# Optimization experiments

Hardware: AMD Instinct MI355X
Metric: run time of the kernel (lower is better)

Reference implementation:

```python
import jax, jax.numpy as jnp
import numpy as np

B, T, IN, H, OUT = 16384, 32, 64, 512, 19


def setup_inputs() -> dict:
    key = jax.random.key(0)
    ks = jax.random.split(key, 10)
    s = 0.05
    return {
        "input_data": jax.random.normal(ks[0], (B, T, IN), dtype=jnp.float32),
        "Wx0": jax.random.normal(ks[1], (IN, 4 * H), dtype=jnp.float32) * s,
        "Wh0": jax.random.normal(ks[2], (H, 4 * H), dtype=jnp.float32) * s,
        "b0": jnp.zeros((4 * H,), dtype=jnp.float32),
        "Wx1": jax.random.normal(ks[3], (H + 1, 4 * H), dtype=jnp.float32) * s,
        "Wh1": jax.random.normal(ks[4], (H, 4 * H), dtype=jnp.float32) * s,
        "b1": jnp.zeros((4 * H,), dtype=jnp.float32),
        "Wlin": jax.random.normal(ks[5], (H, OUT), dtype=jnp.float32) * s,
        "blin": jnp.zeros((OUT,), dtype=jnp.float32),
        "time_step": T,
    }


def _lstm_gates(x, h, c, Wx, Wh, b):
    # PyTorch LSTMCell gate order: i, f, g, o
    g = x @ Wx + h @ Wh + b
    i, f, gc, o = jnp.split(g, 4, axis=-1)
    cn = jax.nn.sigmoid(f) * c + jax.nn.sigmoid(i) * jnp.tanh(gc)
    hn = jax.nn.sigmoid(o) * jnp.tanh(cn)
    return hn, cn


def reference(input_data, Wx0, Wh0, b0, Wx1, Wh1, b1, Wlin, blin, time_step):
    batch = input_data.shape[0]
    hidden = Wh0.shape[0]

    def step(carry, x_t):
        h0, c0, h1, c1 = carry
        flag = x_t[:, :1]  # condition flag in feature column 0
        # cell 1: condition-gated LSTM update
        h0n, c0n = _lstm_gates(x_t, h0, c0, Wx0, Wh0, b0)
        h0 = flag * h0n + (1.0 - flag) * h0
        c0 = flag * c0n + (1.0 - flag) * c0
        # cell 2 input: [flag, h0]
        x2 = jnp.concatenate([flag, h0], axis=1)
        h1n, c1n = _lstm_gates(x2, h1, c1, Wx1, Wh1, b1)
        h1 = flag * h1n + (1.0 - flag) * h1
        c1 = flag * c1n + (1.0 - flag) * c1
        return (h0, c0, h1, c1), None

    z = jnp.zeros((batch, hidden), dtype=input_data.dtype)
    xs = jnp.swapaxes(input_data[:, :time_step, :], 0, 1)  # [T, B, IN]
    (h0, c0, h1, c1), _ = jax.lax.scan(step, (z, z, z, z), xs)
    return h1 @ Wlin + blin
```

## Files before the change

kernel.cpp:

```cpp
#include <hip/hip_runtime.h>
#include <hip/hip_bf16.h>


#define T_STEPS 32
#define IN_F    64
#define HID     512
#define OUT_F   19
#define BW      64

typedef short bf16x8 __attribute__((ext_vector_type(8)));
typedef float f32x4  __attribute__((ext_vector_type(4)));

__device__ __forceinline__ float fast_sig(float x) {
    return __builtin_amdgcn_rcpf(1.0f + __expf(-x));
}
__device__ __forceinline__ float fast_tanh(float x) {
    return 1.0f - 2.0f * __builtin_amdgcn_rcpf(1.0f + __expf(2.0f * x));
}

#define LBAR() do { \
    asm volatile("s_waitcnt lgkmcnt(0)" ::: "memory"); \
    __builtin_amdgcn_sched_barrier(0); \
    __builtin_amdgcn_s_barrier(); \
    __builtin_amdgcn_sched_barrier(0); \
} while (0)

#define MFMA16(A0, A1, A2, A3, Q0, Q1, Q2, Q3) do { \
    acc[0][0] = __builtin_amdgcn_mfma_f32_16x16x32_bf16(A0, Q0, acc[0][0], 0, 0, 0); \
    acc[1][0] = __builtin_amdgcn_mfma_f32_16x16x32_bf16(A1, Q0, acc[1][0], 0, 0, 0); \
    acc[2][0] = __builtin_amdgcn_mfma_f32_16x16x32_bf16(A2, Q0, acc[2][0], 0, 0, 0); \
    acc[3][0] = __builtin_amdgcn_mfma_f32_16x16x32_bf16(A3, Q0, acc[3][0], 0, 0, 0); \
    acc[0][1] = __builtin_amdgcn_mfma_f32_16x16x32_bf16(A0, Q1, acc[0][1], 0, 0, 0); \
    acc[1][1] = __builtin_amdgcn_mfma_f32_16x16x32_bf16(A1, Q1, acc[1][1], 0, 0, 0); \
    acc[2][1] = __builtin_amdgcn_mfma_f32_16x16x32_bf16(A2, Q1, acc[2][1], 0, 0, 0); \
    acc[3][1] = __builtin_amdgcn_mfma_f32_16x16x32_bf16(A3, Q1, acc[3][1], 0, 0, 0); \
    acc[0][2] = __builtin_amdgcn_mfma_f32_16x16x32_bf16(A0, Q2, acc[0][2], 0, 0, 0); \
    acc[1][2] = __builtin_amdgcn_mfma_f32_16x16x32_bf16(A1, Q2, acc[1][2], 0, 0, 0); \
    acc[2][2] = __builtin_amdgcn_mfma_f32_16x16x32_bf16(A2, Q2, acc[2][2], 0, 0, 0); \
    acc[3][2] = __builtin_amdgcn_mfma_f32_16x16x32_bf16(A3, Q2, acc[3][2], 0, 0, 0); \
    acc[0][3] = __builtin_amdgcn_mfma_f32_16x16x32_bf16(A0, Q3, acc[0][3], 0, 0, 0); \
    acc[1][3] = __builtin_amdgcn_mfma_f32_16x16x32_bf16(A1, Q3, acc[1][3], 0, 0, 0); \
    acc[2][3] = __builtin_amdgcn_mfma_f32_16x16x32_bf16(A2, Q3, acc[2][3], 0, 0, 0); \
    acc[3][3] = __builtin_amdgcn_mfma_f32_16x16x32_bf16(A3, Q3, acc[3][3], 0, 0, 0); \
} while (0)

__global__ void wprep_kernel(const float* __restrict__ src,
                             __hip_bfloat16* __restrict__ dst,
                             int kcBits, int rowOff) {
    int idx = blockIdx.x * 256 + threadIdx.x;
    int total = 2048 << (kcBits + 5);
    if (idx >= total) return;
    int e   = idx & 7;
    int lq  = (idx >> 3) & 3;
    int l15 = (idx >> 5) & 15;
    int kc  = (idx >> 9) & ((1 << kcBits) - 1);
    int cb  = idx >> (9 + kcBits);
    int k   = kc * 32 + lq * 8 + e + rowOff;
    int col = cb * 16 + l15;
    dst[idx] = __float2bfloat16(src[(size_t)k * 2048 + col]);
}

template<int KC, int RTS>
__device__ __forceinline__ void gemm_sec4(const char* aE, const char* aO,
                                          const __hip_bfloat16* b0p,
                                          const __hip_bfloat16* b1p,
                                          const __hip_bfloat16* b2p,
                                          const __hip_bfloat16* b3p,
                                          f32x4 acc[4][4]) {
    bf16x8 pa0, pa1, pa2, pa3, pb0, pb1, pb2, pb3, a0, a1, a2, a3;
    pa0 = *(const bf16x8*)(b0p);
    pa1 = *(const bf16x8*)(b1p);
    pa2 = *(const bf16x8*)(b2p);
    pa3 = *(const bf16x8*)(b3p);
    #pragma unroll 1
    for (int m = 0; m < KC - 2; m += 2) {
        const int ao = (m >> 1) * 128;
        pb0 = *(const bf16x8*)(b0p + (m + 1) * 512);
        pb1 = *(const bf16x8*)(b1p + (m + 1) * 512);
        pb2 = *(const bf16x8*)(b2p + (m + 1) * 512);
        pb3 = *(const bf16x8*)(b3p + (m + 1) * 512);
        a0 = *(const bf16x8*)(aE + ao);
        a1 = *(const bf16x8*)(aE + RTS + ao);
        a2 = *(const bf16x8*)(aE + 2 * RTS + ao);
        a3 = *(const bf16x8*)(aE + 3 * RTS + ao);
        MFMA16(a0, a1, a2, a3, pa0, pa1, pa2, pa3);
        pa0 = *(const bf16x8*)(b0p + (m + 2) * 512);
        pa1 = *(const bf16x8*)(b1p + (m + 2) * 512);
        pa2 = *(const bf16x8*)(b2p + (m + 2) * 512);
        pa3 = *(const bf16x8*)(b3p + (m + 2) * 512);
        a0 = *(const bf16x8*)(aO + ao);
        a1 = *(const bf16x8*)(aO + RTS + ao);
        a2 = *(const bf16x8*)(aO + 2 * RTS + ao);
        a3 = *(const bf16x8*)(aO + 3 * RTS + ao);
        MFMA16(a0, a1, a2, a3, pb0, pb1, pb2, pb3);
    }
    {
        const int ao = ((KC - 2) >> 1) * 128;
        pb0 = *(const bf16x8*)(b0p + (KC - 1) * 512);
        pb1 = *(const bf16x8*)(b1p + (KC - 1) * 512);
        pb2 = *(const bf16x8*)(b2p + (KC - 1) * 512);
        pb3 = *(const bf16x8*)(b3p + (KC - 1) * 512);
        a0 = *(const bf16x8*)(aE + ao);
        a1 = *(const bf16x8*)(aE + RTS + ao);
        a2 = *(const bf16x8*)(aE + 2 * RTS + ao);
        a3 = *(const bf16x8*)(aE + 3 * RTS + ao);
        MFMA16(a0, a1, a2, a3, pa0, pa1, pa2, pa3);
        a0 = *(const bf16x8*)(aO + ao);
        a1 = *(const bf16x8*)(aO + RTS + ao);
        a2 = *(const bf16x8*)(aO + 2 * RTS + ao);
        a3 = *(const bf16x8*)(aO + 3 * RTS + ao);
        MFMA16(a0, a1, a2, a3, pb0, pb1, pb2, pb3);
    }
}

__global__ __launch_bounds__(512, 2)
void lstm_main(const float* __restrict__ x,
               const float* __restrict__ b0v,
               const float* __restrict__ Wx1,
               const float* __restrict__ b1v,
               const float* __restrict__ Wlin,
               const float* __restrict__ blin,
               const __hip_bfloat16* __restrict__ Wx0p,
               const __hip_bfloat16* __restrict__ Wh0p,
               const __hip_bfloat16* __restrict__ Wx1hp,
               const __hip_bfloat16* __restrict__ Wh1p,
               float* __restrict__ cws,
               float* __restrict__ hws,
               float* __restrict__ out)
{
    __shared__ __align__(16) __hip_bfloat16 h0s[BW * HID];
    __shared__ __align__(16) __hip_bfloat16 h1s[BW * HID];
    __shared__ __align__(16) __hip_bfloat16 xs[BW * IN_F];
    __shared__ float flags[BW];

    const int tid  = threadIdx.x;
    const int lane = tid & 63;
    const int wid  = tid >> 6;
    const int l15  = lane & 15;
    const int lq   = lane >> 4;
    const int lq16 = lq * 16;
    const int laneoff = l15 * 32 + lq * 8;
    const int asw  = (l15 & 7) << 4;
    const int wg   = blockIdx.x;
    const size_t bbase = (size_t)wg * BW;
    const char* xsC = (const char*)xs;
    const char* h0C = (const char*)h0s;

    const int swE = lq16 ^ asw;
    const int swO = (64 + lq16) ^ asw;
    const char* ahE = h0C + l15 * 1024 + swE;
    const char* ahO = h0C + l15 * 1024 + swO;
    const int h1d = (int)((const char*)h1s - (const char*)h0s);
    const char* axE = xsC + l15 * 128 + swE;
    const char* axO = xsC + l15 * 128 + swO;

    {
        int4 z; z.x = z.y = z.z = z.w = 0;
        int4* p0 = (int4*)h0s; int4* p1 = (int4*)h1s;
        for (int i = tid; i < BW * HID * 2 / 16; i += 512) { p0[i] = z; p1[i] = z; }
    }
    for (int i = tid; i < BW * IN_F; i += 512) {
        int row = i >> 6, k = i & 63;
        float v = __builtin_nontemporal_load(&x[(bbase + row) * (T_STEPS * IN_F) + k]);
        int byte = row * 128 + ((2 * k) ^ ((row & 7) << 4));
        *(__hip_bfloat16*)((char*)xs + byte) = __float2bfloat16(v);
    }
    if (tid < BW) flags[tid] = x[(bbase + tid) * (T_STEPS * IN_F)];
    LBAR();

    const size_t wsWG0 = (size_t)(0 * 256 + wg) * 32768;
    const size_t wsWG1 = (size_t)(1 * 256 + wg) * 32768;

    #pragma unroll 1
    for (int t = 0; t < T_STEPS; ++t) {
        #pragma unroll 1
        for (int sb = 0; sb < 4; ++sb) {
            const int b2 = sb * 8 + wid;
            f32x4 acc[4][4];
            { f32x4 zz = {0.f, 0.f, 0.f, 0.f};
              #pragma unroll
              for (int rt = 0; rt < 4; ++rt)
                  #pragma unroll
                  for (int g = 0; g < 4; ++g) acc[rt][g] = zz; }

            {
                const __hip_bfloat16* bx0 = Wx0p + (size_t)(0 * 32 + b2) * 1024 + laneoff;
                const __hip_bfloat16* bx1 = Wx0p + (size_t)(1 * 32 + b2) * 1024 + laneoff;
                const __hip_bfloat16* bx2 = Wx0p + (size_t)(2 * 32 + b2) * 1024 + laneoff;
                const __hip_bfloat16* bx3 = Wx0p + (size_t)(3 * 32 + b2) * 1024 + laneoff;
                bf16x8 pa0 = *(const bf16x8*)(bx0);
                bf16x8 pa1 = *(const bf16x8*)(bx1);
                bf16x8 pa2 = *(const bf16x8*)(bx2);
                bf16x8 pa3 = *(const bf16x8*)(bx3);
                bf16x8 pb0 = *(const bf16x8*)(bx0 + 512);
                bf16x8 pb1 = *(const bf16x8*)(bx1 + 512);
                bf16x8 pb2 = *(const bf16x8*)(bx2 + 512);
                bf16x8 pb3 = *(const bf16x8*)(bx3 + 512);
                bf16x8 a0 = *(const bf16x8*)(axE);
                bf16x8 a1 = *(const bf16x8*)(axE + 2048);
                bf16x8 a2 = *(const bf16x8*)(axE + 4096);
                bf16x8 a3 = *(const bf16x8*)(axE + 6144);
                MFMA16(a0, a1, a2, a3, pa0, pa1, pa2, pa3);
                a0 = *(const bf16x8*)(axO);
                a1 = *(const bf16x8*)(axO + 2048);
                a2 = *(const bf16x8*)(axO + 4096);
                a3 = *(const bf16x8*)(axO + 6144);
                MFMA16(a0, a1, a2, a3, pb0, pb1, pb2, pb3);
            }
            gemm_sec4<16, 16384>(ahE, ahO,
                Wh0p + (size_t)(0 * 32 + b2) * 8192 + laneoff,
                Wh0p + (size_t)(1 * 32 + b2) * 8192 + laneoff,
                Wh0p + (size_t)(2 * 32 + b2) * 8192 + laneoff,
                Wh0p + (size_t)(3 * 32 + b2) * 8192 + laneoff, acc);

            const size_t sbase = wsWG0 + (size_t)b2 * 1024 + lane * 4;
            const int jcol = b2 * 16 + l15;
            float bia[4];
            #pragma unroll
            for (int g = 0; g < 4; ++g) bia[g] = b0v[g * 512 + jcol];
            #pragma unroll
            for (int rt = 0; rt < 4; ++rt) {
                f32x4 cold, hold;
                if (t > 0) {
                    cold = __builtin_nontemporal_load((const f32x4*)(cws + sbase + rt * 256));
                    hold = *(const f32x4*)(hws + sbase + rt * 256);
                } else {
                    f32x4 zz = {0.f, 0.f, 0.f, 0.f}; cold = zz; hold = zz;
                }
                f32x4 cnew, hnew;
                #pragma unroll
                for (int r = 0; r < 4; ++r) {
                    const float f = flags[rt * 16 + lq * 4 + r];
                    float gi = acc[rt][0][r] + bia[0];
                    float gf = acc[rt][1][r] + bia[1];
                    float gg = acc[rt][2][r] + bia[2];
                    float go = acc[rt][3][r] + bia[3];
                    float cn = fast_sig(gf) * cold[r] + fast_sig(gi) * fast_tanh(gg);
                    float hn = fast_sig(go) * fast_tanh(cn);
                    cnew[r] = f * cn + (1.f - f) * cold[r];
                    hnew[r] = f * hn + (1.f - f) * hold[r];
                }
                __builtin_nontemporal_store(cnew, (f32x4*)(cws + sbase + rt * 256));
                *(f32x4*)(hws + sbase + rt * 256) = hnew;
            }
        }
        __syncthreads();

        for (int i4 = tid; i4 < BW * HID / 4; i4 += 512) {
            f32x4 v = *(const f32x4*)(hws + wsWG0 + (size_t)i4 * 4);
            int lane2 = i4 & 63, rt2 = (i4 >> 6) & 3, b2r = i4 >> 8;
            int col2 = 2 * (b2r * 16 + (lane2 & 15));
            int rowb = rt2 * 16 + (lane2 >> 4) * 4;
            #pragma unroll
            for (int r = 0; r < 4; ++r) {
                int row = rowb + r;
                int byte = row * 1024 + (col2 ^ ((row & 7) << 4));
                *(__hip_bfloat16*)((char*)h0s + byte) = __float2bfloat16(v[r]);
            }
        }
        LBAR();

        #pragma unroll 1
        for (int sb = 0; sb < 4; ++sb) {
            const int b2 = sb * 8 + wid;
            f32x4 acc[4][4];
            { f32x4 zz = {0.f, 0.f, 0.f, 0.f};
              #pragma unroll
              for (int rt = 0; rt < 4; ++rt)
                  #pragma unroll
                  for (int g = 0; g < 4; ++g) acc[rt][g] = zz; }

            gemm_sec4<16, 16384>(ahE, ahO,
                Wx1hp + (size_t)(0 * 32 + b2) * 8192 + laneoff,
                Wx1hp + (size_t)(1 * 32 + b2) * 8192 + laneoff,
                Wx1hp + (size_t)(2 * 32 + b2) * 8192 + laneoff,
                Wx1hp + (size_t)(3 * 32 + b2) * 8192 + laneoff, acc);
            gemm_sec4<16, 16384>(ahE + h1d, ahO + h1d,
                Wh1p + (size_t)(0 * 32 + b2) * 8192 + laneoff,
                Wh1p + (size_t)(1 * 32 + b2) * 8192 + laneoff,
                Wh1p + (size_t)(2 * 32 + b2) * 8192 + laneoff,
                Wh1p + (size_t)(3 * 32 + b2) * 8192 + laneoff, acc);

            const size_t sbase = wsWG1 + (size_t)b2 * 1024 + lane * 4;
            const int jcol = b2 * 16 + l15;
            float bia[4], w10[4];
            #pragma unroll
            for (int g = 0; g < 4; ++g) {
                bia[g] = b1v[g * 512 + jcol];
                w10[g] = Wx1[g * 512 + jcol];
            }
            #pragma unroll
            for (int rt = 0; rt < 4; ++rt) {
                f32x4 cold, hold;
                if (t > 0) {
                    cold = __builtin_nontemporal_load((const f32x4*)(cws + sbase + rt * 256));
                    hold = *(const f32x4*)(hws + sbase + rt * 256);
                } else {
                    f32x4 zz = {0.f, 0.f, 0.f, 0.f}; cold = zz; hold = zz;
                }
                f32x4 cnew, hnew;
                #pragma unroll
                for (int r = 0; r < 4; ++r) {
                    const float f = flags[rt * 16 + lq * 4 + r];
                    float gi = acc[rt][0][r] + bia[0] + f * w10[0];
                    float gf = acc[rt][1][r] + bia[1] + f * w10[1];
                    float gg = acc[rt][2][r] + bia[2] + f * w10[2];
                    float go = acc[rt][3][r] + bia[3] + f * w10[3];
                    float cn = fast_sig(gf) * cold[r] + fast_sig(gi) * fast_tanh(gg);
                    float hn = fast_sig(go) * fast_tanh(cn);
                    cnew[r] = f * cn + (1.f - f) * cold[r];
                    hnew[r] = f * hn + (1.f - f) * hold[r];
                }
                __builtin_nontemporal_store(cnew, (f32x4*)(cws + sbase + rt * 256));
                *(f32x4*)(hws + sbase + rt * 256) = hnew;
            }
        }
        __syncthreads();

        for (int i4 = tid; i4 < BW * HID / 4; i4 += 512) {
            f32x4 v = *(const f32x4*)(hws + wsWG1 + (size_t)i4 * 4);
            int lane2 = i4 & 63, rt2 = (i4 >> 6) & 3, b2r = i4 >> 8;
            int col2 = 2 * (b2r * 16 + (lane2 & 15));
            int rowb = rt2 * 16 + (lane2 >> 4) * 4;
            #pragma unroll
            for (int r = 0; r < 4; ++r) {
                int row = rowb + r;
                int byte = row * 1024 + (col2 ^ ((row & 7) << 4));
                *(__hip_bfloat16*)((char*)h1s + byte) = __float2bfloat16(v[r]);
            }
        }
        if (t + 1 < T_STEPS) {
            for (int i = tid; i < BW * IN_F; i += 512) {
                int row = i >> 6, k = i & 63;
                float v = __builtin_nontemporal_load(&x[(bbase + row) * (T_STEPS * IN_F) + (t + 1) * IN_F + k]);
                int byte = row * 128 + ((2 * k) ^ ((row & 7) << 4));
                *(__hip_bfloat16*)((char*)xs + byte) = __float2bfloat16(v);
            }
            if (tid < BW) flags[tid] = x[(bbase + tid) * (T_STEPS * IN_F) + (t + 1) * IN_F];
        }
        LBAR();
    }

    for (int task = tid; task < BW * OUT_F; task += 512) {
        int o   = task >> 6;
        int row = task & 63;
        float s = blin[o];
        const float* wl = Wlin + o;
        for (int k = 0; k < HID; ++k) {
            int byte = row * 1024 + ((2 * k) ^ ((row & 7) << 4));
            float hv = __bfloat162float(*(const __hip_bfloat16*)((const char*)h1s + byte));
            s += hv * wl[k * OUT_F];
        }
        out[(bbase + row) * OUT_F + o] = s;
    }
}

extern "C" void kernel_launch(void* const* d_in, const int* in_sizes, int n_in,
                              void* d_out, int out_size, void* d_ws, size_t ws_size,
                              hipStream_t stream) {
    const float* x    = (const float*)d_in[0];
    const float* Wx0  = (const float*)d_in[1];
    const float* Wh0  = (const float*)d_in[2];
    const float* b0   = (const float*)d_in[3];
    const float* Wx1  = (const float*)d_in[4];
    const float* Wh1  = (const float*)d_in[5];
    const float* b1   = (const float*)d_in[6];
    const float* Wlin = (const float*)d_in[7];
    const float* blin = (const float*)d_in[8];

    const size_t offWx0p  = 0;
    const size_t offWh0p  = 262144;
    const size_t offWx1hp = 2359296;
    const size_t offWh1p  = 4456448;
    const size_t offC     = 6553600;
    const size_t offH     = 73662464;
    const size_t needed   = 140771328;
    if (ws_size < needed) return;

    char* w = (char*)d_ws;
    __hip_bfloat16* Wx0p  = (__hip_bfloat16*)(w + offWx0p);
    __hip_bfloat16* Wh0p  = (__hip_bfloat16*)(w + offWh0p);
    __hip_bfloat16* Wx1hp = (__hip_bfloat16*)(w + offWx1hp);
    __hip_bfloat16* Wh1p  = (__hip_bfloat16*)(w + offWh1p);
    float* cws = (float*)(w + offC);
    float* hws = (float*)(w + offH);

    dim3 blk(256);
    wprep_kernel<<<(2048 * 64 + 255) / 256, blk, 0, stream>>>(Wx0, Wx0p, 1, 0);
    wprep_kernel<<<(2048 * 512 + 255) / 256, blk, 0, stream>>>(Wh0, Wh0p, 4, 0);
    wprep_kernel<<<(2048 * 512 + 255) / 256, blk, 0, stream>>>(Wx1, Wx1hp, 4, 1);
    wprep_kernel<<<(2048 * 512 + 255) / 256, blk, 0, stream>>>(Wh1, Wh1p, 4, 0);

    lstm_main<<<256, 512, 0, stream>>>(x, b0, Wx1, b1, Wlin, blin,
                                       Wx0p, Wh0p, Wx1hp, Wh1p, cws, hws, (float*)d_out);
}
```

Before: 4.980 ms.

## Skew LSTM layers across timesteps to halve per-step barriers

Restructures the time loop so layer 1 at step t and layer 0 at step t+1 run back to back in one phase, both reading the same h0 buffer, with double-buffered flags. This removes one block-wide barrier and one refill phase per timestep, so each step needs a single sync. The final linear layer now reads fp32 h1 from the workspace instead of the bf16 shared copy, which changes output precision slightly and adds global reads. The prologue and epilogue are unrolled to handle the skew.

```diff
diff --git a/kernel.cpp b/kernel.cpp
--- a/kernel.cpp
+++ b/kernel.cpp
@@ -131,7 +131,8 @@
     __shared__ __align__(16) __hip_bfloat16 h0s[BW * HID];
     __shared__ __align__(16) __hip_bfloat16 h1s[BW * HID];
     __shared__ __align__(16) __hip_bfloat16 xs[BW * IN_F];
-    __shared__ float flags[BW];
+    __shared__ float flags0[BW];
+    __shared__ float flags1[BW];
 
     const int tid  = threadIdx.x;
     const int lane = tid & 63;
@@ -154,25 +155,68 @@
     const char* axE = xsC + l15 * 128 + swE;
     const char* axO = xsC + l15 * 128 + swO;
 
-    {
-        int4 z; z.x = z.y = z.z = z.w = 0;
-        int4* p0 = (int4*)h0s; int4* p1 = (int4*)h1s;
-        for (int i = tid; i < BW * HID * 2 / 16; i += 512) { p0[i] = z; p1[i] = z; }
-    }
-    for (int i = tid; i < BW * IN_F; i += 512) {
-        int row = i >> 6, k = i & 63;
-        float v = __builtin_nontemporal_load(&x[(bbase + row) * (T_STEPS * IN_F) + k]);
-        int byte = row * 128 + ((2 * k) ^ ((row & 7) << 4));
-        *(__hip_bfloat16*)((char*)xs + byte) = __float2bfloat16(v);
-    }
-    if (tid < BW) flags[tid] = x[(bbase + tid) * (T_STEPS * IN_F)];
-    LBAR();
-
     const size_t wsWG0 = (size_t)(0 * 256 + wg) * 32768;
     const size_t wsWG1 = (size_t)(1 * 256 + wg) * 32768;
 
-    #pragma unroll 1
-    for (int t = 0; t < T_STEPS; ++t) {
+    auto do_L1 = [&](bool zstate) {
+        #pragma unroll 1
+        for (int sb = 0; sb < 4; ++sb) {
+            const int b2 = sb * 8 + wid;
+            f32x4 acc[4][4];
+            { f32x4 zz = {0.f, 0.f, 0.f, 0.f};
+              #pragma unroll
+              for (int rt = 0; rt < 4; ++rt)
+                  #pragma unroll
+                  for (int g = 0; g < 4; ++g) acc[rt][g] = zz; }
+
+            gemm_sec4<16, 16384>(ahE, ahO,
+                Wx1hp + (size_t)(0 * 32 + b2) * 8192 + laneoff,
+                Wx1hp + (size_t)(1 * 32 + b2) * 8192 + laneoff,
+                Wx1hp + (size_t)(2 * 32 + b2) * 8192 + laneoff,
+                Wx1hp + (size_t)(3 * 32 + b2) * 8192 + laneoff, acc);
+            gemm_sec4<16, 16384>(ahE + h1d, ahO + h1d,
+                Wh1p + (size_t)(0 * 32 + b2) * 8192 + laneoff,
+                Wh1p + (size_t)(1 * 32 + b2) * 8192 + laneoff,
+                Wh1p + (size_t)(2 * 32 + b2) * 8192 + laneoff,
+                Wh1p + (size_t)(3 * 32 + b2) * 8192 + laneoff, acc);
+
+            const size_t sbase = wsWG1 + (size_t)b2 * 1024 + lane * 4;
+            const int jcol = b2 * 16 + l15;
+            float bia[4], w10[4];
+            #pragma unroll
+            for (int g = 0; g < 4; ++g) {
+                bia[g] = b1v[g * 512 + jcol];
+                w10[g] = Wx1[g * 512 + jcol];
+            }
+            #pragma unroll
+            for (int rt = 0; rt < 4; ++rt) {
+                f32x4 cold, hold;
+                if (!zstate) {
+                    cold = __builtin_nontemporal_load((const f32x4*)(cws + sbase + rt * 256));
+                    hold = *(const f32x4*)(hws + sbase + rt * 256);
+                } else {
+                    f32x4 zz = {0.f, 0.f, 0.f, 0.f}; cold = zz; hold = zz;
+                }
+                f32x4 cnew, hnew;
+                #pragma unroll
+                for (int r = 0; r < 4; ++r) {
+                    const float f = flags0[rt * 16 + lq * 4 + r];
+                    float gi = acc[rt][0][r] + bia[0] + f * w10[0];
+                    float gf = acc[rt][1][r] + bia[1] + f * w10[1];
+                    float gg = acc[rt][2][r] + bia[2] + f * w10[2];
+                    float go = acc[rt][3][r] + bia[3] + f * w10[3];
+                    float cn = fast_sig(gf) * cold[r] + fast_sig(gi) * fast_tanh(gg);
+                    float hn = fast_sig(go) * fast_tanh(cn);
+                    cnew[r] = f * cn + (1.f - f) * cold[r];
+                    hnew[r] = f * hn + (1.f - f) * hold[r];
+                }
+                __builtin_nontemporal_store(cnew, (f32x4*)(cws + sbase + rt * 256));
+                *(f32x4*)(hws + sbase + rt * 256) = hnew;
+            }
+        }
+    };
+
+    auto do_L0 = [&](bool zstate) {
         #pragma unroll 1
         for (int sb = 0; sb < 4; ++sb) {
             const int b2 = sb * 8 + wid;
@@ -221,7 +265,7 @@
             #pragma unroll
             for (int rt = 0; rt < 4; ++rt) {
                 f32x4 cold, hold;
-                if (t > 0) {
+                if (!zstate) {
                     cold = __builtin_nontemporal_load((const f32x4*)(cws + sbase + rt * 256));
                     hold = *(const f32x4*)(hws + sbase + rt * 256);
                 } else {
@@ -230,7 +274,7 @@
                 f32x4 cnew, hnew;
                 #pragma unroll
                 for (int r = 0; r < 4; ++r) {
-                    const float f = flags[rt * 16 + lq * 4 + r];
+                    const float f = flags1[rt * 16 + lq * 4 + r];
                     float gi = acc[rt][0][r] + bia[0];
                     float gf = acc[rt][1][r] + bia[1];
                     float gg = acc[rt][2][r] + bia[2];
@@ -244,10 +288,11 @@
                 *(f32x4*)(hws + sbase + rt * 256) = hnew;
             }
         }
-        __syncthreads();
-
+    };
+
+    auto refill = [&](__hip_bfloat16* dst, size_t wsWG) {
         for (int i4 = tid; i4 < BW * HID / 4; i4 += 512) {
-            f32x4 v = *(const f32x4*)(hws + wsWG0 + (size_t)i4 * 4);
+            f32x4 v = *(const f32x4*)(hws + wsWG + (size_t)i4 * 4);
             int lane2 = i4 & 63, rt2 = (i4 >> 6) & 3, b2r = i4 >> 8;
             int col2 = 2 * (b2r * 16 + (lane2 & 15));
             int rowb = rt2 * 16 + (lane2 >> 4) * 4;
@@ -255,101 +300,72 @@
             for (int r = 0; r < 4; ++r) {
                 int row = rowb + r;
                 int byte = row * 1024 + (col2 ^ ((row & 7) << 4));
-                *(__hip_bfloat16*)((char*)h0s + byte) = __float2bfloat16(v[r]);
+                *(__hip_bfloat16*)((char*)dst + byte) = __float2bfloat16(v[r]);
             }
         }
+    };
+
+    auto stage_x = [&](int tt) {
+        for (int i = tid; i < BW * IN_F; i += 512) {
+            int row = i >> 6, k = i & 63;
+            float v = __builtin_nontemporal_load(&x[(bbase + row) * (T_STEPS * IN_F) + tt * IN_F + k]);
+            int byte = row * 128 + ((2 * k) ^ ((row & 7) << 4));
+            *(__hip_bfloat16*)((char*)xs + byte) = __float2bfloat16(v);
+        }
+    };
+
+    {
+        int4 z; z.x = z.y = z.z = z.w = 0;
+        int4* p0 = (int4*)h0s; int4* p1 = (int4*)h1s;
+        for (int i = tid; i < BW * HID * 2 / 16; i += 512) { p0[i] = z; p1[i] = z; }
+    }
+    stage_x(0);
+    if (tid < BW) {
+        float f0 = x[(bbase + tid) * (T_STEPS * IN_F)];
+        flags0[tid] = f0;
+        flags1[tid] = f0;
+    }
+    LBAR();
+
+    do_L0(true);
+    __syncthreads();
+    refill(h0s, wsWG0);
+    stage_x(1);
+    if (tid < BW) flags1[tid] = x[(bbase + tid) * (T_STEPS * IN_F) + IN_F];
+    LBAR();
+
+    #pragma unroll 1
+    for (int t = 0; t < T_STEPS - 1; ++t) {
+        do_L1(t == 0);
+        do_L0(false);
+        __syncthreads();
+        refill(h0s, wsWG0);
+        refill(h1s, wsWG1);
+        if (tid < BW) {
+            float f1 = flags1[tid];
+            flags0[tid] = f1;
+            flags1[tid] = (t + 2 < T_STEPS)
+                ? x[(bbase + tid) * (T_STEPS * IN_F) + (size_t)(t + 2) * IN_F] : 0.f;
+        }
+        if (t + 2 < T_STEPS) stage_x(t + 2);
         LBAR();
-
-        #pragma unroll 1
-        for (int sb = 0; sb < 4; ++sb) {
-            const int b2 = sb * 8 + wid;
-            f32x4 acc[4][4];
-            { f32x4 zz = {0.f, 0.f, 0.f, 0.f};
-              #pragma unroll
-              for (int rt = 0; rt < 4; ++rt)
-                  #pragma unroll
-                  for (int g = 0; g < 4; ++g) acc[rt][g] = zz; }
-
-            gemm_sec4<16, 16384>(ahE, ahO,
-                Wx1hp + (size_t)(0 * 32 + b2) * 8192 + laneoff,
-                Wx1hp + (size_t)(1 * 32 + b2) * 8192 + laneoff,
-                Wx1hp + (size_t)(2 * 32 + b2) * 8192 + laneoff,
-                Wx1hp + (size_t)(3 * 32 + b2) * 8192 + laneoff, acc);
-            gemm_sec4<16, 16384>(ahE + h1d, ahO + h1d,
-                Wh1p + (size_t)(0 * 32 + b2) * 8192 + laneoff,
-                Wh1p + (size_t)(1 * 32 + b2) * 8192 + laneoff,
-                Wh1p + (size_t)(2 * 32 + b2) * 8192 + laneoff,
-                Wh1p + (size_t)(3 * 32 + b2) * 8192 + laneoff, acc);
-
-            const size_t sbase = wsWG1 + (size_t)b2 * 1024 + lane * 4;
-            const int jcol = b2 * 16 + l15;
-            float bia[4], w10[4];
-            #pragma unroll
-            for (int g = 0; g < 4; ++g) {
-                bia[g] = b1v[g * 512 + jcol];
-                w10[g] = Wx1[g * 512 + jcol];
-            }
-            #pragma unroll
-            for (int rt = 0; rt < 4; ++rt) {
-                f32x4 cold, hold;
-                if (t > 0) {
-                    cold = __builtin_nontemporal_load((const f32x4*)(cws + sbase + rt * 256));
-                    hold = *(const f32x4*)(hws + sbase + rt * 256);
-                } else {
-                    f32x4 zz = {0.f, 0.f, 0.f, 0.f}; cold = zz; hold = zz;
-                }
-                f32x4 cnew, hnew;
-                #pragma unroll
-                for (int r = 0; r < 4; ++r) {
-                    const float f = flags[rt * 16 + lq * 4 + r];
-                    float gi = acc[rt][0][r] + bia[0] + f * w10[0];
-                    float gf = acc[rt][1][r] + bia[1] + f * w10[1];
-                    float gg = acc[rt][2][r] + bia[2] + f * w10[2];
-                    float go = acc[rt][3][r] + bia[3] + f * w10[3];
-                    float cn = fast_sig(gf) * cold[r] + fast_sig(gi) * fast_tanh(gg);
-                    float hn = fast_sig(go) * fast_tanh(cn);
-                    cnew[r] = f * cn + (1.f - f) * cold[r];
-                    hnew[r] = f * hn + (1.f - f) * hold[r];
-                }
-                __builtin_nontemporal_store(cnew, (f32x4*)(cws + sbase + rt * 256));
-                *(f32x4*)(hws + sbase + rt * 256) = hnew;
-            }
-        }
-        __syncthreads();
-
-        for (int i4 = tid; i4 < BW * HID / 4; i4 += 512) {
-            f32x4 v = *(const f32x4*)(hws + wsWG1 + (size_t)i4 * 4);
-            int lane2 = i4 & 63, rt2 = (i4 >> 6) & 3, b2r = i4 >> 8;
-            int col2 = 2 * (b2r * 16 + (lane2 & 15));
-            int rowb = rt2 * 16 + (lane2 >> 4) * 4;
-            #pragma unroll
-            for (int r = 0; r < 4; ++r) {
-                int row = rowb + r;
-                int byte = row * 1024 + (col2 ^ ((row & 7) << 4));
-                *(__hip_bfloat16*)((char*)h1s + byte) = __float2bfloat16(v[r]);
-            }
-        }
-        if (t + 1 < T_STEPS) {
-            for (int i = tid; i < BW * IN_F; i += 512) {
-                int row = i >> 6, k = i & 63;
-                float v = __builtin_nontemporal_load(&x[(bbase + row) * (T_STEPS * IN_F) + (t + 1) * IN_F + k]);
-                int byte = row * 128 + ((2 * k) ^ ((row & 7) << 4));
-                *(__hip_bfloat16*)((char*)xs + byte) = __float2bfloat16(v);
-            }
-            if (tid < BW) flags[tid] = x[(bbase + tid) * (T_STEPS * IN_F) + (t + 1) * IN_F];
-        }
-        LBAR();
-    }
+    }
+
+    do_L1(false);
+    __syncthreads();
 
     for (int task = tid; task < BW * OUT_F; task += 512) {
         int o   = task >> 6;
         int row = task & 63;
+        const int base_row = ((row >> 4) << 8) + (((row >> 2) & 3) << 6) + (row & 3);
         float s = blin[o];
+        const float* hp = hws + wsWG1 + base_row;
         const float* wl = Wlin + o;
-        for (int k = 0; k < HID; ++k) {
-            int byte = row * 1024 + ((2 * k) ^ ((row & 7) << 4));
-            float hv = __bfloat162float(*(const __hip_bfloat16*)((const char*)h1s + byte));
-            s += hv * wl[k * OUT_F];
+        #pragma unroll 1
+        for (int kb = 0; kb < 32; ++kb) {
+            #pragma unroll
+            for (int kl = 0; kl < 16; ++kl)
+                s += hp[kb * 1024 + kl * 4] * wl[(kb * 16 + kl) * OUT_F];
         }
         out[(bbase + row) * OUT_F + o] = s;
     }
```

New measurement: 5.014 ms. No clear change (+0.7%).
